# Kernel optimization log

Hardware: AMD Instinct MI355X
Metric: run time of the kernel (lower is better)

## Reference

```python
import jax, jax.numpy as jnp
import numpy as np

DIM = 256
H = 4
HD = DIM // H          # head_dim = 64
B = 4
N = 2048
M = 3                  # number of modalities
TEMP = 0.07
EPS = 1e-5             # torch LayerNorm eps


def _layernorm(x, g, b):
    mu = jnp.mean(x, axis=-1, keepdims=True)
    var = jnp.var(x, axis=-1, keepdims=True)  # biased, matches torch
    return (x - mu) / jnp.sqrt(var + EPS) * g + b


def setup_inputs() -> dict:
    key = jax.random.key(0)
    ks = jax.random.split(key, 8)
    s = 0.02
    return {
        "m0": jax.random.normal(ks[0], (B, N, DIM), jnp.float32),
        "m1": jax.random.normal(ks[1], (B, N, DIM), jnp.float32),
        "m2": jax.random.normal(ks[2], (B, N, DIM), jnp.float32),
        # torch Linear weights are [out, in]; applied as x @ W.T
        "Wq": jax.random.normal(ks[3], (DIM, DIM), jnp.float32) * s,
        "Wk": jax.random.normal(ks[4], (DIM, DIM), jnp.float32) * s,
        "Wv": jax.random.normal(ks[5], (DIM, DIM), jnp.float32) * s,
        "g1": jnp.ones((DIM,), jnp.float32),
        "be1": jnp.zeros((DIM,), jnp.float32),
        "W1": jax.random.normal(ks[6], (4 * DIM, DIM), jnp.float32) * s,
        "bm1": jnp.zeros((4 * DIM,), jnp.float32),
        "W2": jax.random.normal(ks[7], (DIM, 4 * DIM), jnp.float32) * s,
        "bm2": jnp.zeros((DIM,), jnp.float32),
        "g2": jnp.ones((DIM,), jnp.float32),
        "be2": jnp.zeros((DIM,), jnp.float32),
    }


def reference(m0, m1, m2, Wq, Wk, Wv, g1, be1, W1, bm1, W2, bm2, g2, be2):
    mods = jnp.stack([m0, m1, m2])  # [M, B, N, D]

    def proj(W):
        # x @ W.T, split heads -> [M, B, H, N, HD]
        y = jnp.einsum('mbnd,ed->mbne', mods, W)
        return y.reshape(M, B, N, H, HD).transpose(0, 1, 3, 2, 4)

    q, k, v = proj(Wq), proj(Wk), proj(Wv)
    scale = 1.0 / np.sqrt(HD).astype(np.float32)

    pair_loss = jnp.float32(0.0)
    updates = []
    for i in range(M):  # small fixed modality loop
        upd = jnp.zeros((B, N, DIM), mods.dtype)
        for j in range(M):
            # [B, H, N, N] cross-modal scores
            sim = jnp.einsum('bhnd,bhmd->bhnm', q[i], k[j]) * scale
            attn = jax.nn.softmax(sim, axis=-1)
            if i != j:
                diag = jnp.diagonal(sim, axis1=-2, axis2=-1)      # [B, H, N]
                lse = jax.nn.logsumexp(sim / TEMP, axis=-1)       # [B, H, N]
                pair_loss = pair_loss + jnp.mean(-diag + lse)
            au = jnp.einsum('bhnm,bhmd->bhnd', attn, v[j])
            upd = upd + au.transpose(0, 2, 1, 3).reshape(B, N, DIM)
        updates.append(upd)

    # original accumulates the pairwise loss once per outer modality, each
    # time divided by M*(M-1)  ->  total = M * pair_loss / (M*(M-1))
    total_loss = M * pair_loss / (M * (M - 1))

    outs = []
    for m in range(M):
        x = mods[m] + updates[m]
        x = _layernorm(x, g1, be1)
        h = jax.nn.gelu(x @ W1.T + bm1, approximate=False)  # exact GELU like torch
        x = x + (h @ W2.T + bm2)
        x = _layernorm(x, g2, be2)
        outs.append(x)

    return (outs[0], outs[1], outs[2], total_loss)
```

## Files before the change

kernel.cpp:

```cpp
#include <hip/hip_runtime.h>


typedef float f32x4 __attribute__((ext_vector_type(4)));
typedef float f32x16 __attribute__((ext_vector_type(16)));
typedef __bf16 bf16x8 __attribute__((ext_vector_type(8)));
typedef unsigned int u32x4 __attribute__((ext_vector_type(4)));
typedef unsigned short bfu4 __attribute__((ext_vector_type(4)));
typedef unsigned short bfu;

#define MFMA(a, b, c) __builtin_amdgcn_mfma_f32_16x16x32_bf16(a, b, c, 0, 0, 0)
#define MFMA32(a, b, c) __builtin_amdgcn_mfma_f32_32x32x16_bf16(a, b, c, 0, 0, 0)

#define NTOK 2048
#define DIMM 256
#define HDIM 64
#define DFF 1024
#define OUT_LOSS 6291456
#define INVT 14.285714285714286f

__device__ __forceinline__ bfu f2bf(float f) {
  unsigned u = __float_as_uint(f);
  u += 0x7FFFu + ((u >> 16) & 1u);
  return (bfu)(u >> 16);
}

__device__ __forceinline__ bf16x8 ldfrag(const bfu* p) {
  return __builtin_bit_cast(bf16x8, *reinterpret_cast<const u32x4*>(p));
}

__device__ __forceinline__ unsigned pkbf(float lo, float hi) {
  unsigned d;
  asm("v_cvt_pk_bf16_f32 %0, %1, %2" : "=v"(d) : "v"(lo), "v"(hi));
  return d;
}
__device__ __forceinline__ void swap32u(unsigned& a, unsigned& b) {
  asm("v_permlane32_swap_b32 %0, %1" : "+v"(a), "+v"(b));
}
__device__ __forceinline__ float red32_add(float x) {
  float y = x;
  asm("v_permlane32_swap_b32 %0, %1" : "+v"(x), "+v"(y));
  return x + y;
}
__device__ __forceinline__ float red32_max(float x) {
  float y = x;
  asm("v_permlane32_swap_b32 %0, %1" : "+v"(x), "+v"(y));
  return fmaxf(x, y);
}

__global__ __launch_bounds__(256) void k_cvt(const float* __restrict__ src,
                                             bfu* __restrict__ dst, int n4) {
  int idx = blockIdx.x * 256 + threadIdx.x;
  if (idx < n4) {
    f32x4 v = reinterpret_cast<const f32x4*>(src)[idx];
    bfu4 o;
    o[0] = f2bf(v[0]); o[1] = f2bf(v[1]); o[2] = f2bf(v[2]); o[3] = f2bf(v[3]);
    reinterpret_cast<bfu4*>(dst)[idx] = o;
  }
}


#define RROW(r) (((r) & 3) + 8 * ((r) >> 2) + 4 * hi)

__global__ __launch_bounds__(256) void k_proj(const bfu* __restrict__ Xb,
                                              const bfu* __restrict__ Wcat,
                                              bfu* __restrict__ Qb,
                                              bfu* __restrict__ Kb,
                                              bfu* __restrict__ VTb) {
  __shared__ __align__(16) bfu sA[128][72];
  __shared__ __align__(16) bfu sB[128][72];
  const int tid = threadIdx.x;
  const int lane = tid & 63, w = tid >> 6;
  const int l31 = lane & 31, hi = lane >> 5, hi8 = hi * 8;
  const int wm = w >> 1, wn = w & 1;
  const int row0 = blockIdx.x * 128;
  const int col0 = blockIdx.y * 128;
  const bfu* Ap = Xb + (size_t)row0 * 256;
  const bfu* Bp = Wcat + (size_t)col0 * 256;
  f32x16 acc00 = {}, acc01 = {}, acc10 = {}, acc11 = {};
  u32x4 rA[4], rB[4];
#pragma unroll
  for (int t = 0; t < 4; ++t) {
    const int c = tid + 256 * t;
    rA[t] = *reinterpret_cast<const u32x4*>(Ap + (size_t)(c >> 3) * 256 + (c & 7) * 8);
    rB[t] = *reinterpret_cast<const u32x4*>(Bp + (size_t)(c >> 3) * 256 + (c & 7) * 8);
  }
#pragma unroll
  for (int ks = 0; ks < 4; ++ks) {
    __syncthreads();
#pragma unroll
    for (int t = 0; t < 4; ++t) {
      const int c = tid + 256 * t;
      *reinterpret_cast<u32x4*>(&sA[c >> 3][(c & 7) * 8]) = rA[t];
      *reinterpret_cast<u32x4*>(&sB[c >> 3][(c & 7) * 8]) = rB[t];
    }
    __syncthreads();
    if (ks < 3) {
      const int k0 = (ks + 1) * 64;
#pragma unroll
      for (int t = 0; t < 4; ++t) {
        const int c = tid + 256 * t;
        rA[t] = *reinterpret_cast<const u32x4*>(Ap + (size_t)(c >> 3) * 256 + k0 + (c & 7) * 8);
        rB[t] = *reinterpret_cast<const u32x4*>(Bp + (size_t)(c >> 3) * 256 + k0 + (c & 7) * 8);
      }
    }
#pragma unroll
    for (int kk = 0; kk < 4; ++kk) {
      bf16x8 a0 = ldfrag(&sA[wm * 64 + l31][kk * 16 + hi8]);
      bf16x8 a1 = ldfrag(&sA[wm * 64 + 32 + l31][kk * 16 + hi8]);
      bf16x8 b0 = ldfrag(&sB[wn * 64 + l31][kk * 16 + hi8]);
      bf16x8 b1 = ldfrag(&sB[wn * 64 + 32 + l31][kk * 16 + hi8]);
      acc00 = MFMA32(a0, b0, acc00);
      acc01 = MFMA32(a0, b1, acc01);
      acc10 = MFMA32(a1, b0, acc10);
      acc11 = MFMA32(a1, b1, acc11);
    }
  }
  const int mb = row0 >> 11;
  const int cb = col0 + wn * 64;
  const int which = cb >> 8;
  const int h = (cb >> 6) & 3;
  const size_t obase = ((size_t)mb * 4 + h) * ((size_t)NTOK * HDIM);
  const int tokb = (row0 & 2047) + wm * 64;
  const float qs = (which == 0) ? 0.125f : 1.0f;
#define STORE_QK(ACC, MT, NT)                                                 \
  {                                                                           \
    bfu* dst = (which ? Kb : Qb) + obase;                                     \
    _Pragma("unroll") for (int r = 0; r < 16; ++r) {                          \
      const int tok = tokb + (MT) * 32 + RROW(r);                             \
      dst[(size_t)tok * 64 + (NT) * 32 + l31] = f2bf((ACC)[r] * qs);          \
    }                                                                         \
  }
#define STORE_VT(ACC, MT, NT)                                                 \
  {                                                                           \
    _Pragma("unroll") for (int g = 0; g < 4; ++g) {                           \
      bfu4 pk;                                                                \
      _Pragma("unroll") for (int q = 0; q < 4; ++q) pk[q] = f2bf((ACC)[4 * g + q]); \
      const int tok = tokb + (MT) * 32 + 8 * g + 4 * hi;                      \
      *reinterpret_cast<bfu4*>(                                               \
          &VTb[obase + (size_t)((NT) * 32 + l31) * NTOK + tok]) = pk;         \
    }                                                                         \
  }
  if (which < 2) {
    STORE_QK(acc00, 0, 0) STORE_QK(acc01, 0, 1)
    STORE_QK(acc10, 1, 0) STORE_QK(acc11, 1, 1)
  } else {
    STORE_VT(acc00, 0, 0) STORE_VT(acc01, 0, 1)
    STORE_VT(acc10, 1, 0) STORE_VT(acc11, 1, 1)
  }
}

__global__ __launch_bounds__(256) void k_ffn1(const bfu* __restrict__ x1b,
                                              const bfu* __restrict__ W1b,
                                              const float* __restrict__ bm1,
                                              bfu* __restrict__ hb) {
  __shared__ __align__(16) bfu sA[128][72];
  __shared__ __align__(16) bfu sB[128][72];
  const int tid = threadIdx.x;
  const int lane = tid & 63, w = tid >> 6;
  const int l31 = lane & 31, hi = lane >> 5, hi8 = hi * 8;
  const int wm = w >> 1, wn = w & 1;
  const int row0 = blockIdx.x * 128;
  const int col0 = blockIdx.y * 128;
  const bfu* Ap = x1b + (size_t)row0 * 256;
  const bfu* Bp = W1b + (size_t)col0 * 256;
  f32x16 acc00 = {}, acc01 = {}, acc10 = {}, acc11 = {};
  u32x4 rA[4], rB[4];
#pragma unroll
  for (int t = 0; t < 4; ++t) {
    const int c = tid + 256 * t;
    rA[t] = *reinterpret_cast<const u32x4*>(Ap + (size_t)(c >> 3) * 256 + (c & 7) * 8);
    rB[t] = *reinterpret_cast<const u32x4*>(Bp + (size_t)(c >> 3) * 256 + (c & 7) * 8);
  }
#pragma unroll
  for (int ks = 0; ks < 4; ++ks) {
    __syncthreads();
#pragma unroll
    for (int t = 0; t < 4; ++t) {
      const int c = tid + 256 * t;
      *reinterpret_cast<u32x4*>(&sA[c >> 3][(c & 7) * 8]) = rA[t];
      *reinterpret_cast<u32x4*>(&sB[c >> 3][(c & 7) * 8]) = rB[t];
    }
    __syncthreads();
    if (ks < 3) {
      const int k0 = (ks + 1) * 64;
#pragma unroll
      for (int t = 0; t < 4; ++t) {
        const int c = tid + 256 * t;
        rA[t] = *reinterpret_cast<const u32x4*>(Ap + (size_t)(c >> 3) * 256 + k0 + (c & 7) * 8);
        rB[t] = *reinterpret_cast<const u32x4*>(Bp + (size_t)(c >> 3) * 256 + k0 + (c & 7) * 8);
      }
    }
#pragma unroll
    for (int kk = 0; kk < 4; ++kk) {
      bf16x8 a0 = ldfrag(&sA[wm * 64 + l31][kk * 16 + hi8]);
      bf16x8 a1 = ldfrag(&sA[wm * 64 + 32 + l31][kk * 16 + hi8]);
      bf16x8 b0 = ldfrag(&sB[wn * 64 + l31][kk * 16 + hi8]);
      bf16x8 b1 = ldfrag(&sB[wn * 64 + 32 + l31][kk * 16 + hi8]);
      acc00 = MFMA32(a0, b0, acc00);
      acc01 = MFMA32(a0, b1, acc01);
      acc10 = MFMA32(a1, b0, acc10);
      acc11 = MFMA32(a1, b1, acc11);
    }
  }
  const int tokb = row0 + wm * 64;
#define STORE_H(ACC, MT, NT)                                                  \
  {                                                                           \
    const int e = col0 + wn * 64 + (NT) * 32 + l31;                           \
    const float bias = bm1[e];                                                \
    _Pragma("unroll") for (int r = 0; r < 16; ++r) {                          \
      const int tok = tokb + (MT) * 32 + RROW(r);                             \
      float v = (ACC)[r] + bias;                                              \
      v = 0.5f * v * (1.0f + erff(v * 0.70710678118f));                       \
      hb[(size_t)tok * DFF + e] = f2bf(v);                                    \
    }                                                                         \
  }
  STORE_H(acc00, 0, 0) STORE_H(acc01, 0, 1)
  STORE_H(acc10, 1, 0) STORE_H(acc11, 1, 1)
}

__global__ __launch_bounds__(256) void k_ffn2(const bfu* __restrict__ hb,
                                              const bfu* __restrict__ W2b,
                                              const float* __restrict__ bm2,
                                              const float* __restrict__ x1f,
                                              float* __restrict__ x2f) {
  __shared__ __align__(16) bfu sA[128][72];
  __shared__ __align__(16) bfu sB[64][72];
  const int tid = threadIdx.x;
  const int lane = tid & 63, w = tid >> 6;
  const int l31 = lane & 31, hi = lane >> 5, hi8 = hi * 8;
  const int row0 = blockIdx.x * 128;
  const int col0 = blockIdx.y * 64;
  const bfu* Ap = hb + (size_t)row0 * DFF;
  const bfu* Bp = W2b + (size_t)col0 * DFF;
  f32x16 acc0 = {}, acc1 = {};
  u32x4 rA[4], rB[2];
#pragma unroll
  for (int t = 0; t < 4; ++t) {
    const int c = tid + 256 * t;
    rA[t] = *reinterpret_cast<const u32x4*>(Ap + (size_t)(c >> 3) * DFF + (c & 7) * 8);
  }
#pragma unroll
  for (int t = 0; t < 2; ++t) {
    const int c = tid + 256 * t;
    rB[t] = *reinterpret_cast<const u32x4*>(Bp + (size_t)(c >> 3) * DFF + (c & 7) * 8);
  }
  for (int ks = 0; ks < 16; ++ks) {
    __syncthreads();
#pragma unroll
    for (int t = 0; t < 4; ++t) {
      const int c = tid + 256 * t;
      *reinterpret_cast<u32x4*>(&sA[c >> 3][(c & 7) * 8]) = rA[t];
    }
#pragma unroll
    for (int t = 0; t < 2; ++t) {
      const int c = tid + 256 * t;
      *reinterpret_cast<u32x4*>(&sB[c >> 3][(c & 7) * 8]) = rB[t];
    }
    __syncthreads();
    if (ks < 15) {
      const int k0 = (ks + 1) * 64;
#pragma unroll
      for (int t = 0; t < 4; ++t) {
        const int c = tid + 256 * t;
        rA[t] = *reinterpret_cast<const u32x4*>(Ap + (size_t)(c >> 3) * DFF + k0 + (c & 7) * 8);
      }
#pragma unroll
      for (int t = 0; t < 2; ++t) {
        const int c = tid + 256 * t;
        rB[t] = *reinterpret_cast<const u32x4*>(Bp + (size_t)(c >> 3) * DFF + k0 + (c & 7) * 8);
      }
    }
#pragma unroll
    for (int kk = 0; kk < 4; ++kk) {
      bf16x8 a = ldfrag(&sA[w * 32 + l31][kk * 16 + hi8]);
      bf16x8 b0 = ldfrag(&sB[l31][kk * 16 + hi8]);
      bf16x8 b1 = ldfrag(&sB[32 + l31][kk * 16 + hi8]);
      acc0 = MFMA32(a, b0, acc0);
      acc1 = MFMA32(a, b1, acc1);
    }
  }
  const int tokb = row0 + w * 32;
#define STORE_Y(ACC, NT)                                                      \
  {                                                                           \
    const int e = col0 + (NT) * 32 + l31;                                     \
    const float bias = bm2[e];                                                \
    _Pragma("unroll") for (int r = 0; r < 16; ++r) {                          \
      const int tok = tokb + RROW(r);                                         \
      x2f[(size_t)tok * DIMM + e] =                                           \
          (ACC)[r] + bias + x1f[(size_t)tok * DIMM + e];                      \
    }                                                                         \
  }
  STORE_Y(acc0, 0) STORE_Y(acc1, 1)
}

__global__ __launch_bounds__(256, 3) void k_attn(const bfu* __restrict__ Qb,
                                                 const bfu* __restrict__ Kb,
                                                 const bfu* __restrict__ VTb,
                                                 float* __restrict__ upd,
                                                 float* __restrict__ lossbuf) {
  __shared__ __align__(16) bfu sK[2][64][72];
  __shared__ __align__(16) bfu sV[2][64][72];
  __shared__ float sRed[4];
  const int tid = threadIdx.x;
  const int lane = tid & 63, w = tid >> 6;
  const int l31 = lane & 31, hi = lane >> 5;
  const int hi8 = hi * 8;
  const int qt = blockIdx.x, bh = blockIdx.y, i = blockIdx.z;
  const int b = bh >> 2, h = bh & 3;
  const int q0 = qt * 128 + w * 32;
  const int q = q0 + l31;
  const int ktd = q0 >> 6;
  const size_t plane = (size_t)NTOK * HDIM;
  const size_t qoff = (((size_t)i * 4 + b) * 4 + h) * plane;
  const int r0 = tid >> 2, c0 = (tid & 3) * 2;

  bf16x8 qf[4];
#pragma unroll
  for (int c = 0; c < 4; ++c)
    qf[c] = ldfrag(Qb + qoff + (size_t)q * HDIM + c * 16 + hi8);

  const size_t ubase = (((size_t)i * 4 + b) * NTOK) * DIMM;
  float* up = upd + ubase + (size_t)q * DIMM + h * 64;
  float lossacc = 0.0f;
  f32x16 uac0 = {}, uac1 = {};

  for (int j = 0; j < 3; ++j) {
    const size_t kvoff = (((size_t)j * 4 + b) * 4 + h) * plane;
    const bfu* Kp = Kb + kvoff;
    const bfu* Vp = VTb + kvoff;
    const bool wl = (i != j);
    float mrun = -1e30f, lrun = 0.0f, l2run = 0.0f;
    f32x16 O0 = {}, O1 = {};
    u32x4 pk0, pk1, pv0, pv1;

#define ISSUE_TILE(K0)                                                       \
    {                                                                        \
      const bfu* kp_ = Kp + (size_t)((K0) + r0) * HDIM + c0 * 8;             \
      pk0 = *reinterpret_cast<const u32x4*>(kp_);                            \
      pk1 = *reinterpret_cast<const u32x4*>(kp_ + 8);                        \
      const bfu* vp_ = Vp + (size_t)r0 * NTOK + (K0) + c0 * 8;               \
      pv0 = *reinterpret_cast<const u32x4*>(vp_);                            \
      pv1 = *reinterpret_cast<const u32x4*>(vp_ + 8);                        \
    }
#define WRITE_TILE(BUF)                                                      \
    {                                                                        \
      *reinterpret_cast<u32x4*>(&sK[BUF][r0][c0 * 8]) = pk0;                 \
      *reinterpret_cast<u32x4*>(&sK[BUF][r0][c0 * 8 + 8]) = pk1;             \
      *reinterpret_cast<u32x4*>(&sV[BUF][r0][c0 * 8]) = pv0;                 \
      *reinterpret_cast<u32x4*>(&sV[BUF][r0][c0 * 8 + 8]) = pv1;             \
    }

    ISSUE_TILE(0);
    WRITE_TILE(0);
    __syncthreads();
    int cur = 0;

    for (int kt = 0; kt < 32; ++kt) {
      if (kt < 31) ISSUE_TILE((kt + 1) * 64);

      f32x16 S0 = {}, S1 = {};
      __builtin_amdgcn_s_setprio(1);
#pragma unroll
      for (int c = 0; c < 4; ++c) {
        bf16x8 a0 = ldfrag(&sK[cur][l31][c * 16 + hi8]);
        bf16x8 a1 = ldfrag(&sK[cur][32 + l31][c * 16 + hi8]);
        S0 = MFMA32(a0, qf[c], S0);
        S1 = MFMA32(a1, qf[c], S1);
      }
      __builtin_amdgcn_s_setprio(0);

      if (wl && kt == ktd) {
#pragma unroll
        for (int r = 0; r < 16; ++r) {
          const int klow = (r & 3) + 8 * (r >> 2) + 4 * hi;
          const float sv = (w & 1) ? S1[r] : S0[r];
          if (klow == l31) lossacc -= sv;
        }
      }

      float pmax = -1e30f;
#pragma unroll
      for (int r = 0; r < 16; ++r) pmax = fmaxf(pmax, fmaxf(S0[r], S1[r]));
      pmax = red32_max(pmax);
      if (__any(pmax > mrun + 1.9f)) {
        const float mnew = fmaxf(mrun, pmax);
        const float al = __expf(mrun - mnew);
        const float a2 = __expf((mrun - mnew) * INVT);
        O0 *= al; O1 *= al;
        lrun *= al; l2run *= a2;
        mrun = mnew;
      }
      float ps = 0.0f, p2s = 0.0f;
#pragma unroll
      for (int r = 0; r < 16; ++r) {
        const float t0 = S0[r] - mrun, t1 = S1[r] - mrun;
        const float e0 = __expf(t0), e1 = __expf(t1);
        ps += e0 + e1;
        if (wl) p2s += __expf(t0 * INVT) + __expf(t1 * INVT);
        S0[r] = e0; S1[r] = e1;
      }
      lrun += red32_add(ps);
      if (wl) l2run += red32_add(p2s);

      u32x4 Bc[4];
#pragma unroll
      for (int half = 0; half < 2; ++half) {
#pragma unroll
        for (int sub = 0; sub < 2; ++sub) {
          unsigned q01, q23, q45, q67;
          if (half == 0) {
            q01 = pkbf(S0[sub * 8 + 0], S0[sub * 8 + 1]);
            q23 = pkbf(S0[sub * 8 + 2], S0[sub * 8 + 3]);
            q45 = pkbf(S0[sub * 8 + 4], S0[sub * 8 + 5]);
            q67 = pkbf(S0[sub * 8 + 6], S0[sub * 8 + 7]);
          } else {
            q01 = pkbf(S1[sub * 8 + 0], S1[sub * 8 + 1]);
            q23 = pkbf(S1[sub * 8 + 2], S1[sub * 8 + 3]);
            q45 = pkbf(S1[sub * 8 + 4], S1[sub * 8 + 5]);
            q67 = pkbf(S1[sub * 8 + 6], S1[sub * 8 + 7]);
          }
          swap32u(q01, q45);
          swap32u(q23, q67);
          u32x4 bb; bb[0] = q01; bb[1] = q23; bb[2] = q45; bb[3] = q67;
          Bc[half * 2 + sub] = bb;
        }
      }

      __builtin_amdgcn_s_setprio(1);
#pragma unroll
      for (int c = 0; c < 4; ++c) {
        const bf16x8 pb = __builtin_bit_cast(bf16x8, Bc[c]);
        bf16x8 a0 = ldfrag(&sV[cur][l31][c * 16 + hi8]);
        bf16x8 a1 = ldfrag(&sV[cur][32 + l31][c * 16 + hi8]);
        O0 = MFMA32(a0, pb, O0);
        O1 = MFMA32(a1, pb, O1);
      }
      __builtin_amdgcn_s_setprio(0);

      __syncthreads();
      if (kt < 31) {
        WRITE_TILE(cur ^ 1);
        __syncthreads();
        cur ^= 1;
      }
    }

    const float inv = 1.0f / lrun;
    uac0 += O0 * inv;
    uac1 += O1 * inv;
    if (wl && hi == 0)
      lossacc += mrun * INVT + __logf(l2run);
  }

#pragma unroll
  for (int g = 0; g < 4; ++g) {
    f32x4 v0, v1;
#pragma unroll
    for (int q2 = 0; q2 < 4; ++q2) {
      v0[q2] = uac0[4 * g + q2];
      v1[q2] = uac1[4 * g + q2];
    }
    *reinterpret_cast<f32x4*>(up + 8 * g + 4 * hi) = v0;
    *reinterpret_cast<f32x4*>(up + 32 + 8 * g + 4 * hi) = v1;
  }
  float v = lossacc;
#pragma unroll
  for (int mk = 1; mk < 64; mk <<= 1) v += __shfl_xor(v, mk);
  if (lane == 0) sRed[w] = v;
  __syncthreads();
  if (tid == 0)
    lossbuf[((size_t)i * 16 + bh) * 16 + qt] =
        sRed[0] + sRed[1] + sRed[2] + sRed[3];
}

__global__ __launch_bounds__(256) void k_ln1(const float* __restrict__ m0,
                                             const float* __restrict__ m1,
                                             const float* __restrict__ m2,
                                             const float* __restrict__ upd,
                                             const float* __restrict__ g1,
                                             const float* __restrict__ be1,
                                             float* __restrict__ x1f,
                                             bfu* __restrict__ x1b) {
  const int tid = threadIdx.x;
  const int lane = tid & 63, w = tid >> 6;
  const int row = blockIdx.x * 4 + w;
  const int m = row >> 13;
  const int rr = row & 8191;
  const float* src = (m == 0 ? m0 : (m == 1 ? m1 : m2)) + (size_t)rr * DIMM;
  f32x4 x = *reinterpret_cast<const f32x4*>(src + lane * 4);
  f32x4 u = *reinterpret_cast<const f32x4*>(upd + (size_t)row * DIMM + lane * 4);
  x += u;
  float s = x[0] + x[1] + x[2] + x[3];
  float s2 = x[0] * x[0] + x[1] * x[1] + x[2] * x[2] + x[3] * x[3];
#pragma unroll
  for (int mk = 1; mk < 64; mk <<= 1) { s += __shfl_xor(s, mk); s2 += __shfl_xor(s2, mk); }
  const float mu = s * (1.0f / 256.0f);
  const float var = s2 * (1.0f / 256.0f) - mu * mu;
  const float rstd = rsqrtf(var + 1e-5f);
  f32x4 g = *reinterpret_cast<const f32x4*>(g1 + lane * 4);
  f32x4 bb = *reinterpret_cast<const f32x4*>(be1 + lane * 4);
  f32x4 o;
#pragma unroll
  for (int qi = 0; qi < 4; ++qi) o[qi] = (x[qi] - mu) * rstd * g[qi] + bb[qi];
  *reinterpret_cast<f32x4*>(x1f + (size_t)row * DIMM + lane * 4) = o;
  bfu4 ob;
#pragma unroll
  for (int qi = 0; qi < 4; ++qi) ob[qi] = f2bf(o[qi]);
  *reinterpret_cast<bfu4*>(x1b + (size_t)row * DIMM + lane * 4) = ob;
}

__global__ __launch_bounds__(256) void k_ln2(const float* __restrict__ x2f,
                                             const float* __restrict__ g2,
                                             const float* __restrict__ be2,
                                             float* __restrict__ out) {
  const int tid = threadIdx.x;
  const int lane = tid & 63, w = tid >> 6;
  const int row = blockIdx.x * 4 + w;
  f32x4 x = *reinterpret_cast<const f32x4*>(x2f + (size_t)row * DIMM + lane * 4);
  float s = x[0] + x[1] + x[2] + x[3];
  float s2 = x[0] * x[0] + x[1] * x[1] + x[2] * x[2] + x[3] * x[3];
#pragma unroll
  for (int mk = 1; mk < 64; mk <<= 1) { s += __shfl_xor(s, mk); s2 += __shfl_xor(s2, mk); }
  const float mu = s * (1.0f / 256.0f);
  const float var = s2 * (1.0f / 256.0f) - mu * mu;
  const float rstd = rsqrtf(var + 1e-5f);
  f32x4 g = *reinterpret_cast<const f32x4*>(g2 + lane * 4);
  f32x4 bb = *reinterpret_cast<const f32x4*>(be2 + lane * 4);
  f32x4 o;
#pragma unroll
  for (int qi = 0; qi < 4; ++qi) o[qi] = (x[qi] - mu) * rstd * g[qi] + bb[qi];
  *reinterpret_cast<f32x4*>(out + (size_t)row * DIMM + lane * 4) = o;
}

__global__ __launch_bounds__(256) void k_loss(const float* __restrict__ lossbuf,
                                              float* __restrict__ out) {
  __shared__ float red[4];
  const int tid = threadIdx.x;
  float s = 0.0f;
  for (int idx = tid; idx < 768; idx += 256) s += lossbuf[idx];
#pragma unroll
  for (int mk = 1; mk < 64; mk <<= 1) s += __shfl_xor(s, mk);
  if ((tid & 63) == 0) red[tid >> 6] = s;
  __syncthreads();
  if (tid == 0)
    out[OUT_LOSS] = (red[0] + red[1] + red[2] + red[3]) * (1.0f / (32768.0f * 2.0f));
}

extern "C" void kernel_launch(void* const* d_in, const int* in_sizes, int n_in,
                              void* d_out, int out_size, void* d_ws, size_t ws_size,
                              hipStream_t stream) {
  const float* m0 = (const float*)d_in[0];
  const float* m1 = (const float*)d_in[1];
  const float* m2 = (const float*)d_in[2];
  const float* Wq = (const float*)d_in[3];
  const float* Wk = (const float*)d_in[4];
  const float* Wv = (const float*)d_in[5];
  const float* g1 = (const float*)d_in[6];
  const float* be1 = (const float*)d_in[7];
  const float* W1 = (const float*)d_in[8];
  const float* bm1 = (const float*)d_in[9];
  const float* W2 = (const float*)d_in[10];
  const float* bm2 = (const float*)d_in[11];
  const float* g2 = (const float*)d_in[12];
  const float* be2 = (const float*)d_in[13];
  float* out = (float*)d_out;

  char* ws = (char*)d_ws;
  bfu* Xb   = (bfu*)(ws + 0);
  bfu* Wqkv = (bfu*)(ws + 12582912);
  bfu* Qb   = (bfu*)(ws + 12976128);
  bfu* Kb   = (bfu*)(ws + 25559040);
  bfu* VTb  = (bfu*)(ws + 38141952);
  bfu* Hb   = (bfu*)(ws + 0);
  float* upd  = (float*)(ws + 50724864);
  float* x2f  = (float*)(ws + 50724864);
  float* x1f  = (float*)(ws + 75890688);
  bfu* x1b    = (bfu*)(ws + 101056512);
  bfu* W1b    = (bfu*)(ws + 113639424);
  bfu* W2b    = (bfu*)(ws + 114163712);
  float* lossbuf = (float*)(ws + 114688000);

  k_cvt<<<2048, 256, 0, stream>>>(m0, Xb, 524288);
  k_cvt<<<2048, 256, 0, stream>>>(m1, Xb + 2097152, 524288);
  k_cvt<<<2048, 256, 0, stream>>>(m2, Xb + 4194304, 524288);
  k_cvt<<<64, 256, 0, stream>>>(Wq, Wqkv, 16384);
  k_cvt<<<64, 256, 0, stream>>>(Wk, Wqkv + 65536, 16384);
  k_cvt<<<64, 256, 0, stream>>>(Wv, Wqkv + 131072, 16384);
  k_cvt<<<256, 256, 0, stream>>>(W1, W1b, 65536);
  k_cvt<<<256, 256, 0, stream>>>(W2, W2b, 65536);

  k_proj<<<dim3(192, 6), 256, 0, stream>>>(Xb, Wqkv, Qb, Kb, VTb);
  k_attn<<<dim3(16, 16, 3), 256, 0, stream>>>(Qb, Kb, VTb, upd, lossbuf);
  k_ln1<<<6144, 256, 0, stream>>>(m0, m1, m2, upd, g1, be1, x1f, x1b);
  k_ffn1<<<dim3(192, 8), 256, 0, stream>>>(x1b, W1b, bm1, Hb);
  k_ffn2<<<dim3(192, 4), 256, 0, stream>>>(Hb, W2b, bm2, x1f, x2f);
  k_ln2<<<6144, 256, 0, stream>>>(x2f, g2, be2, out);
  k_loss<<<1, 256, 0, stream>>>(lossbuf, out);
}
```

Before: 372.0 us.

## Split attention grid over modality pairs, use exp2 softmax and bf16 intermediates

The attention kernel now launches one block per (i,j) modality pair instead of looping over j inside a block, tripling the grid to raise occupancy and parallelism. Each pair writes its normalized output in bf16 to a separate buffer, and LN1 sums the three. Q is pre-scaled by log2(e) so the softmax can use native exp2/log2, with the loss terms rescaled by ln2 to compensate. The LN1 fp32 output buffer is dropped and FFN2 reads the bf16 residual instead. These lose some precision and add extra bf16 update traffic, and the K/V shared-memory double buffering is removed.

```diff
diff --git a/kernel.cpp b/kernel.cpp
--- a/kernel.cpp
+++ b/kernel.cpp
@@ -4,6 +4,7 @@
 typedef float f32x4 __attribute__((ext_vector_type(4)));
 typedef float f32x16 __attribute__((ext_vector_type(16)));
 typedef __bf16 bf16x8 __attribute__((ext_vector_type(8)));
+typedef unsigned int u32x2 __attribute__((ext_vector_type(2)));
 typedef unsigned int u32x4 __attribute__((ext_vector_type(4)));
 typedef unsigned short bfu4 __attribute__((ext_vector_type(4)));
 typedef unsigned short bfu;
@@ -17,11 +18,19 @@
 #define DFF 1024
 #define OUT_LOSS 6291456
 #define INVT 14.285714285714286f
+#define LN2F 0.6931471805599453f
+#define LOG2EF 1.4426950408889634f
+
+#define EXP2F(x) __builtin_amdgcn_exp2f(x)
+#define LOG2F(x) __builtin_amdgcn_logf(x)
 
 __device__ __forceinline__ bfu f2bf(float f) {
   unsigned u = __float_as_uint(f);
   u += 0x7FFFu + ((u >> 16) & 1u);
   return (bfu)(u >> 16);
+}
+__device__ __forceinline__ float frombf(bfu v) {
+  return __uint_as_float(((unsigned)v) << 16);
 }
 
 __device__ __forceinline__ bf16x8 ldfrag(const bfu* p) {
@@ -57,7 +66,6 @@
     reinterpret_cast<bfu4*>(dst)[idx] = o;
   }
 }
-
 
 #define RROW(r) (((r) & 3) + 8 * ((r) >> 2) + 4 * hi)
 
@@ -121,7 +129,7 @@
   const int h = (cb >> 6) & 3;
   const size_t obase = ((size_t)mb * 4 + h) * ((size_t)NTOK * HDIM);
   const int tokb = (row0 & 2047) + wm * 64;
-  const float qs = (which == 0) ? 0.125f : 1.0f;
+  const float qs = (which == 0) ? 0.125f * LOG2EF : 1.0f;
 #define STORE_QK(ACC, MT, NT)                                                 \
   {                                                                           \
     bfu* dst = (which ? Kb : Qb) + obase;                                     \
@@ -221,7 +229,7 @@
 __global__ __launch_bounds__(256) void k_ffn2(const bfu* __restrict__ hb,
                                               const bfu* __restrict__ W2b,
                                               const float* __restrict__ bm2,
-                                              const float* __restrict__ x1f,
+                                              const bfu* __restrict__ x1b,
                                               float* __restrict__ x2f) {
   __shared__ __align__(16) bfu sA[128][72];
   __shared__ __align__(16) bfu sB[64][72];
@@ -287,7 +295,7 @@
     _Pragma("unroll") for (int r = 0; r < 16; ++r) {                          \
       const int tok = tokb + RROW(r);                                         \
       x2f[(size_t)tok * DIMM + e] =                                           \
-          (ACC)[r] + bias + x1f[(size_t)tok * DIMM + e];                      \
+          (ACC)[r] + bias + frombf(x1b[(size_t)tok * DIMM + e]);              \
     }                                                                         \
   }
   STORE_Y(acc0, 0) STORE_Y(acc1, 1)
@@ -296,22 +304,27 @@
 __global__ __launch_bounds__(256, 3) void k_attn(const bfu* __restrict__ Qb,
                                                  const bfu* __restrict__ Kb,
                                                  const bfu* __restrict__ VTb,
-                                                 float* __restrict__ upd,
+                                                 bfu* __restrict__ upd3,
                                                  float* __restrict__ lossbuf) {
-  __shared__ __align__(16) bfu sK[2][64][72];
-  __shared__ __align__(16) bfu sV[2][64][72];
+  __shared__ __align__(16) bfu sK[64][72];
+  __shared__ __align__(16) bfu sV[64][72];
   __shared__ float sRed[4];
   const int tid = threadIdx.x;
   const int lane = tid & 63, w = tid >> 6;
   const int l31 = lane & 31, hi = lane >> 5;
   const int hi8 = hi * 8;
-  const int qt = blockIdx.x, bh = blockIdx.y, i = blockIdx.z;
+  const int qt = blockIdx.x, bh = blockIdx.y, ij = blockIdx.z;
+  const int i = ij / 3, j = ij % 3;
+  const bool wl = (i != j);
   const int b = bh >> 2, h = bh & 3;
   const int q0 = qt * 128 + w * 32;
   const int q = q0 + l31;
   const int ktd = q0 >> 6;
   const size_t plane = (size_t)NTOK * HDIM;
   const size_t qoff = (((size_t)i * 4 + b) * 4 + h) * plane;
+  const size_t kvoff = (((size_t)j * 4 + b) * 4 + h) * plane;
+  const bfu* Kp = Kb + kvoff;
+  const bfu* Vp = VTb + kvoff;
   const int r0 = tid >> 2, c0 = (tid & 3) * 2;
 
   bf16x8 qf[4];
@@ -319,19 +332,10 @@
   for (int c = 0; c < 4; ++c)
     qf[c] = ldfrag(Qb + qoff + (size_t)q * HDIM + c * 16 + hi8);
 
-  const size_t ubase = (((size_t)i * 4 + b) * NTOK) * DIMM;
-  float* up = upd + ubase + (size_t)q * DIMM + h * 64;
   float lossacc = 0.0f;
-  f32x16 uac0 = {}, uac1 = {};
-
-  for (int j = 0; j < 3; ++j) {
-    const size_t kvoff = (((size_t)j * 4 + b) * 4 + h) * plane;
-    const bfu* Kp = Kb + kvoff;
-    const bfu* Vp = VTb + kvoff;
-    const bool wl = (i != j);
-    float mrun = -1e30f, lrun = 0.0f, l2run = 0.0f;
-    f32x16 O0 = {}, O1 = {};
-    u32x4 pk0, pk1, pv0, pv1;
+  float mrun = -1e30f, lrun = 0.0f, l2run = 0.0f;
+  f32x16 O0 = {}, O1 = {};
+  u32x4 pk0, pk1, pv0, pv1;
 
 #define ISSUE_TILE(K0)                                                       \
     {                                                                        \
@@ -342,154 +346,153 @@
       pv0 = *reinterpret_cast<const u32x4*>(vp_);                            \
       pv1 = *reinterpret_cast<const u32x4*>(vp_ + 8);                        \
     }
-#define WRITE_TILE(BUF)                                                      \
+#define WRITE_TILE()                                                         \
     {                                                                        \
-      *reinterpret_cast<u32x4*>(&sK[BUF][r0][c0 * 8]) = pk0;                 \
-      *reinterpret_cast<u32x4*>(&sK[BUF][r0][c0 * 8 + 8]) = pk1;             \
-      *reinterpret_cast<u32x4*>(&sV[BUF][r0][c0 * 8]) = pv0;                 \
-      *reinterpret_cast<u32x4*>(&sV[BUF][r0][c0 * 8 + 8]) = pv1;             \
-    }
-
-    ISSUE_TILE(0);
-    WRITE_TILE(0);
-    __syncthreads();
-    int cur = 0;
-
-    for (int kt = 0; kt < 32; ++kt) {
-      if (kt < 31) ISSUE_TILE((kt + 1) * 64);
-
-      f32x16 S0 = {}, S1 = {};
-      __builtin_amdgcn_s_setprio(1);
-#pragma unroll
-      for (int c = 0; c < 4; ++c) {
-        bf16x8 a0 = ldfrag(&sK[cur][l31][c * 16 + hi8]);
-        bf16x8 a1 = ldfrag(&sK[cur][32 + l31][c * 16 + hi8]);
-        S0 = MFMA32(a0, qf[c], S0);
-        S1 = MFMA32(a1, qf[c], S1);
+      *reinterpret_cast<u32x4*>(&sK[r0][c0 * 8]) = pk0;                      \
+      *reinterpret_cast<u32x4*>(&sK[r0][c0 * 8 + 8]) = pk1;                  \
+      *reinterpret_cast<u32x4*>(&sV[r0][c0 * 8]) = pv0;                      \
+      *reinterpret_cast<u32x4*>(&sV[r0][c0 * 8 + 8]) = pv1;                  \
+    }
+
+  ISSUE_TILE(0);
+  WRITE_TILE();
+  __syncthreads();
+
+  for (int kt = 0; kt < 32; ++kt) {
+    if (kt < 31) ISSUE_TILE((kt + 1) * 64);
+
+    f32x16 S0 = {}, S1 = {};
+    __builtin_amdgcn_s_setprio(1);
+#pragma unroll
+    for (int c = 0; c < 4; ++c) {
+      bf16x8 a0 = ldfrag(&sK[l31][c * 16 + hi8]);
+      bf16x8 a1 = ldfrag(&sK[32 + l31][c * 16 + hi8]);
+      S0 = MFMA32(a0, qf[c], S0);
+      S1 = MFMA32(a1, qf[c], S1);
+    }
+    __builtin_amdgcn_s_setprio(0);
+
+    if (wl && kt == ktd) {
+#pragma unroll
+      for (int r = 0; r < 16; ++r) {
+        const int klow = (r & 3) + 8 * (r >> 2) + 4 * hi;
+        const float sv = (w & 1) ? S1[r] : S0[r];
+        if (klow == l31) lossacc -= sv * LN2F;
       }
-      __builtin_amdgcn_s_setprio(0);
-
-      if (wl && kt == ktd) {
-#pragma unroll
-        for (int r = 0; r < 16; ++r) {
-          const int klow = (r & 3) + 8 * (r >> 2) + 4 * hi;
-          const float sv = (w & 1) ? S1[r] : S0[r];
-          if (klow == l31) lossacc -= sv;
+    }
+
+    float pmax = -1e30f;
+#pragma unroll
+    for (int r = 0; r < 16; ++r) pmax = fmaxf(pmax, fmaxf(S0[r], S1[r]));
+    pmax = red32_max(pmax);
+    if (__any(pmax > mrun + 1.9f)) {
+      const float mnew = fmaxf(mrun, pmax);
+      const float al = EXP2F(mrun - mnew);
+      const float a2 = EXP2F((mrun - mnew) * INVT);
+      O0 *= al; O1 *= al;
+      lrun *= al; l2run *= a2;
+      mrun = mnew;
+    }
+    float psA = 0.0f, psB = 0.0f, p2A = 0.0f, p2B = 0.0f;
+#pragma unroll
+    for (int r = 0; r < 16; ++r) {
+      const float t0 = S0[r] - mrun, t1 = S1[r] - mrun;
+      const float e0 = EXP2F(t0), e1 = EXP2F(t1);
+      psA += e0; psB += e1;
+      if (wl) { p2A += EXP2F(t0 * INVT); p2B += EXP2F(t1 * INVT); }
+      S0[r] = e0; S1[r] = e1;
+    }
+    lrun += red32_add(psA + psB);
+    if (wl) l2run += red32_add(p2A + p2B);
+
+    u32x4 Bc[4];
+#pragma unroll
+    for (int half = 0; half < 2; ++half) {
+#pragma unroll
+      for (int sub = 0; sub < 2; ++sub) {
+        unsigned q01, q23, q45, q67;
+        if (half == 0) {
+          q01 = pkbf(S0[sub * 8 + 0], S0[sub * 8 + 1]);
+          q23 = pkbf(S0[sub * 8 + 2], S0[sub * 8 + 3]);
+          q45 = pkbf(S0[sub * 8 + 4], S0[sub * 8 + 5]);
+          q67 = pkbf(S0[sub * 8 + 6], S0[sub * 8 + 7]);
+        } else {
+          q01 = pkbf(S1[sub * 8 + 0], S1[sub * 8 + 1]);
+          q23 = pkbf(S1[sub * 8 + 2], S1[sub * 8 + 3]);
+          q45 = pkbf(S1[sub * 8 + 4], S1[sub * 8 + 5]);
+          q67 = pkbf(S1[sub * 8 + 6], S1[sub * 8 + 7]);
         }
+        swap32u(q01, q45);
+        swap32u(q23, q67);
+        u32x4 bb; bb[0] = q01; bb[1] = q23; bb[2] = q45; bb[3] = q67;
+        Bc[half * 2 + sub] = bb;
       }
-
-      float pmax = -1e30f;
-#pragma unroll
-      for (int r = 0; r < 16; ++r) pmax = fmaxf(pmax, fmaxf(S0[r], S1[r]));
-      pmax = red32_max(pmax);
-      if (__any(pmax > mrun + 1.9f)) {
-        const float mnew = fmaxf(mrun, pmax);
-        const float al = __expf(mrun - mnew);
-        const float a2 = __expf((mrun - mnew) * INVT);
-        O0 *= al; O1 *= al;
-        lrun *= al; l2run *= a2;
-        mrun = mnew;
-      }
-      float ps = 0.0f, p2s = 0.0f;
-#pragma unroll
-      for (int r = 0; r < 16; ++r) {
-        const float t0 = S0[r] - mrun, t1 = S1[r] - mrun;
-        const float e0 = __expf(t0), e1 = __expf(t1);
-        ps += e0 + e1;
-        if (wl) p2s += __expf(t0 * INVT) + __expf(t1 * INVT);
-        S0[r] = e0; S1[r] = e1;
-      }
-      lrun += red32_add(ps);
-      if (wl) l2run += red32_add(p2s);
-
-      u32x4 Bc[4];
-#pragma unroll
-      for (int half = 0; half < 2; ++half) {
-#pragma unroll
-        for (int sub = 0; sub < 2; ++sub) {
-          unsigned q01, q23, q45, q67;
-          if (half == 0) {
-            q01 = pkbf(S0[sub * 8 + 0], S0[sub * 8 + 1]);
-            q23 = pkbf(S0[sub * 8 + 2], S0[sub * 8 + 3]);
-            q45 = pkbf(S0[sub * 8 + 4], S0[sub * 8 + 5]);
-            q67 = pkbf(S0[sub * 8 + 6], S0[sub * 8 + 7]);
-          } else {
-            q01 = pkbf(S1[sub * 8 + 0], S1[sub * 8 + 1]);
-            q23 = pkbf(S1[sub * 8 + 2], S1[sub * 8 + 3]);
-            q45 = pkbf(S1[sub * 8 + 4], S1[sub * 8 + 5]);
-            q67 = pkbf(S1[sub * 8 + 6], S1[sub * 8 + 7]);
-          }
-          swap32u(q01, q45);
-          swap32u(q23, q67);
-          u32x4 bb; bb[0] = q01; bb[1] = q23; bb[2] = q45; bb[3] = q67;
-          Bc[half * 2 + sub] = bb;
-        }
-      }
-
-      __builtin_amdgcn_s_setprio(1);
-#pragma unroll
-      for (int c = 0; c < 4; ++c) {
-        const bf16x8 pb = __builtin_bit_cast(bf16x8, Bc[c]);
-        bf16x8 a0 = ldfrag(&sV[cur][l31][c * 16 + hi8]);
-        bf16x8 a1 = ldfrag(&sV[cur][32 + l31][c * 16 + hi8]);
-        O0 = MFMA32(a0, pb, O0);
-        O1 = MFMA32(a1, pb, O1);
-      }
-      __builtin_amdgcn_s_setprio(0);
-
+    }
+
+    __builtin_amdgcn_s_setprio(1);
+#pragma unroll
+    for (int c = 0; c < 4; ++c) {
+      const bf16x8 pb = __builtin_bit_cast(bf16x8, Bc[c]);
+      bf16x8 a0 = ldfrag(&sV[l31][c * 16 + hi8]);
+      bf16x8 a1 = ldfrag(&sV[32 + l31][c * 16 + hi8]);
+      O0 = MFMA32(a0, pb, O0);
+      O1 = MFMA32(a1, pb, O1);
+    }
+    __builtin_amdgcn_s_setprio(0);
+
+    __syncthreads();
+    if (kt < 31) {
+      WRITE_TILE();
       __syncthreads();
-      if (kt < 31) {
-        WRITE_TILE(cur ^ 1);
-        __syncthreads();
-        cur ^= 1;
-      }
-    }
-
-    const float inv = 1.0f / lrun;
-    uac0 += O0 * inv;
-    uac1 += O1 * inv;
-    if (wl && hi == 0)
-      lossacc += mrun * INVT + __logf(l2run);
-  }
-
+    }
+  }
+
+  const float inv = 1.0f / lrun;
+  bfu* up = upd3 + ((size_t)((j * 3 + i) * 4 + b) * NTOK + q) * DIMM + h * 64;
 #pragma unroll
   for (int g = 0; g < 4; ++g) {
-    f32x4 v0, v1;
-#pragma unroll
-    for (int q2 = 0; q2 < 4; ++q2) {
-      v0[q2] = uac0[4 * g + q2];
-      v1[q2] = uac1[4 * g + q2];
-    }
-    *reinterpret_cast<f32x4*>(up + 8 * g + 4 * hi) = v0;
-    *reinterpret_cast<f32x4*>(up + 32 + 8 * g + 4 * hi) = v1;
-  }
+    u32x2 st0, st1;
+    st0[0] = pkbf(O0[4 * g + 0] * inv, O0[4 * g + 1] * inv);
+    st0[1] = pkbf(O0[4 * g + 2] * inv, O0[4 * g + 3] * inv);
+    st1[0] = pkbf(O1[4 * g + 0] * inv, O1[4 * g + 1] * inv);
+    st1[1] = pkbf(O1[4 * g + 2] * inv, O1[4 * g + 3] * inv);
+    *reinterpret_cast<u32x2*>(up + 8 * g + 4 * hi) = st0;
+    *reinterpret_cast<u32x2*>(up + 32 + 8 * g + 4 * hi) = st1;
+  }
+  if (wl && hi == 0)
+    lossacc += LN2F * (mrun * INVT + LOG2F(l2run));
+
   float v = lossacc;
 #pragma unroll
   for (int mk = 1; mk < 64; mk <<= 1) v += __shfl_xor(v, mk);
   if (lane == 0) sRed[w] = v;
   __syncthreads();
   if (tid == 0)
-    lossbuf[((size_t)i * 16 + bh) * 16 + qt] =
+    lossbuf[((size_t)ij * 16 + bh) * 16 + qt] =
         sRed[0] + sRed[1] + sRed[2] + sRed[3];
 }
 
 __global__ __launch_bounds__(256) void k_ln1(const float* __restrict__ m0,
                                              const float* __restrict__ m1,
                                              const float* __restrict__ m2,
-                                             const float* __restrict__ upd,
+                                             const bfu* __restrict__ upd3,
                                              const float* __restrict__ g1,
                                              const float* __restrict__ be1,
-                                             float* __restrict__ x1f,
                                              bfu* __restrict__ x1b) {
   const int tid = threadIdx.x;
   const int lane = tid & 63, w = tid >> 6;
   const int row = blockIdx.x * 4 + w;
-  const int m = row >> 13;
+  const int i = row >> 13;
   const int rr = row & 8191;
-  const float* src = (m == 0 ? m0 : (m == 1 ? m1 : m2)) + (size_t)rr * DIMM;
+  const float* src = (i == 0 ? m0 : (i == 1 ? m1 : m2)) + (size_t)rr * DIMM;
   f32x4 x = *reinterpret_cast<const f32x4*>(src + lane * 4);
-  f32x4 u = *reinterpret_cast<const f32x4*>(upd + (size_t)row * DIMM + lane * 4);
-  x += u;
+#pragma unroll
+  for (int j = 0; j < 3; ++j) {
+    bfu4 uv = *reinterpret_cast<const bfu4*>(
+        upd3 + ((size_t)(j * 3 + i) * 8192 + rr) * DIMM + lane * 4);
+#pragma unroll
+    for (int qi = 0; qi < 4; ++qi) x[qi] += frombf(uv[qi]);
+  }
   float s = x[0] + x[1] + x[2] + x[3];
   float s2 = x[0] * x[0] + x[1] * x[1] + x[2] * x[2] + x[3] * x[3];
 #pragma unroll
@@ -499,13 +502,10 @@
   const float rstd = rsqrtf(var + 1e-5f);
   f32x4 g = *reinterpret_cast<const f32x4*>(g1 + lane * 4);
   f32x4 bb = *reinterpret_cast<const f32x4*>(be1 + lane * 4);
-  f32x4 o;
-#pragma unroll
-  for (int qi = 0; qi < 4; ++qi) o[qi] = (x[qi] - mu) * rstd * g[qi] + bb[qi];
-  *reinterpret_cast<f32x4*>(x1f + (size_t)row * DIMM + lane * 4) = o;
   bfu4 ob;
 #pragma unroll
-  for (int qi = 0; qi < 4; ++qi) ob[qi] = f2bf(o[qi]);
+  for (int qi = 0; qi < 4; ++qi)
+    ob[qi] = f2bf((x[qi] - mu) * rstd * g[qi] + bb[qi]);
   *reinterpret_cast<bfu4*>(x1b + (size_t)row * DIMM + lane * 4) = ob;
 }
 
@@ -537,7 +537,7 @@
   __shared__ float red[4];
   const int tid = threadIdx.x;
   float s = 0.0f;
-  for (int idx = tid; idx < 768; idx += 256) s += lossbuf[idx];
+  for (int idx = tid; idx < 2304; idx += 256) s += lossbuf[idx];
 #pragma unroll
   for (int mk = 1; mk < 64; mk <<= 1) s += __shfl_xor(s, mk);
   if ((tid & 63) == 0) red[tid >> 6] = s;
@@ -572,13 +572,12 @@
   bfu* Kb   = (bfu*)(ws + 25559040);
   bfu* VTb  = (bfu*)(ws + 38141952);
   bfu* Hb   = (bfu*)(ws + 0);
-  float* upd  = (float*)(ws + 50724864);
-  float* x2f  = (float*)(ws + 50724864);
-  float* x1f  = (float*)(ws + 75890688);
-  bfu* x1b    = (bfu*)(ws + 101056512);
-  bfu* W1b    = (bfu*)(ws + 113639424);
-  bfu* W2b    = (bfu*)(ws + 114163712);
-  float* lossbuf = (float*)(ws + 114688000);
+  bfu* upd3 = (bfu*)(ws + 50724864);
+  float* x2f = (float*)(ws + 50724864);
+  bfu* x1b  = (bfu*)(ws + 88473600);
+  bfu* W1b  = (bfu*)(ws + 101056512);
+  bfu* W2b  = (bfu*)(ws + 101580800);
+  float* lossbuf = (float*)(ws + 102105088);
 
   k_cvt<<<2048, 256, 0, stream>>>(m0, Xb, 524288);
   k_cvt<<<2048, 256, 0, stream>>>(m1, Xb + 2097152, 524288);
@@ -590,10 +589,10 @@
   k_cvt<<<256, 256, 0, stream>>>(W2, W2b, 65536);
 
   k_proj<<<dim3(192, 6), 256, 0, stream>>>(Xb, Wqkv, Qb, Kb, VTb);
-  k_attn<<<dim3(16, 16, 3), 256, 0, stream>>>(Qb, Kb, VTb, upd, lossbuf);
-  k_ln1<<<6144, 256, 0, stream>>>(m0, m1, m2, upd, g1, be1, x1f, x1b);
+  k_attn<<<dim3(16, 16, 9), 256, 0, stream>>>(Qb, Kb, VTb, upd3, lossbuf);
+  k_ln1<<<6144, 256, 0, stream>>>(m0, m1, m2, upd3, g1, be1, x1b);
   k_ffn1<<<dim3(192, 8), 256, 0, stream>>>(x1b, W1b, bm1, Hb);
-  k_ffn2<<<dim3(192, 4), 256, 0, stream>>>(Hb, W2b, bm2, x1f, x2f);
+  k_ffn2<<<dim3(192, 4), 256, 0, stream>>>(Hb, W2b, bm2, x1b, x2f);
   k_ln2<<<6144, 256, 0, stream>>>(x2f, g2, be2, out);
   k_loss<<<1, 256, 0, stream>>>(lossbuf, out);
 }
```

Measured after the change: 337.2 us. 1.1x faster.
